# Kernel optimization log

Measured on AMD Instinct MI355X. Metric: run time of the kernel, lower is better.

## Reference

```python
import jax, jax.numpy as jnp
import numpy as np

N = 50000      # nodes
E = 800000     # edges
IN = 128       # in_channels
HID = 64       # hidden_channels
HEADS = 4
OUT = 2        # out_channels


def setup_inputs() -> dict:
    key = jax.random.key(0)
    ks = jax.random.split(key, 14)
    p = lambda k, shape: 0.1 * jax.random.normal(k, shape, dtype=jnp.float32)
    x = jax.random.normal(ks[0], (N, IN), dtype=jnp.float32)
    edge_index = jax.random.randint(ks[1], (2, E), 0, N, dtype=jnp.int64)
    return {
        'x': x, 'edge_index': edge_index,
        'W1': p(ks[2], (IN, HEADS * HID)), 'a_src1': p(ks[3], (HEADS, HID)),
        'a_dst1': p(ks[4], (HEADS, HID)), 'b1': p(ks[5], (HEADS * HID,)),
        'W2': p(ks[6], (HEADS * HID, HID)), 'a_src2': p(ks[7], (1, HID)),
        'a_dst2': p(ks[8], (1, HID)), 'b2': p(ks[9], (HID,)),
        'Wm1': p(ks[10], (2 * HID, HID)), 'bm1': p(ks[11], (HID,)),
        'Wm2': p(ks[12], (HID, OUT)), 'bm2': p(ks[13], (OUT,)),
    }


def _gat_conv(x, src, dst, W, a_src, a_dst, b, heads, out_c, concat):
    """PyG GATConv (eval mode): linear -> per-edge leakyrelu score ->
    segment softmax over destination -> scatter-sum aggregation."""
    n = x.shape[0]
    h = (x @ W).reshape(n, heads, out_c)                 # [N,H,C]
    s_src = jnp.einsum('nhc,hc->nh', h, a_src)           # [N,H]
    s_dst = jnp.einsum('nhc,hc->nh', h, a_dst)           # [N,H]
    e = jax.nn.leaky_relu(s_src[src] + s_dst[dst], 0.2)  # [E,H]
    m = jax.ops.segment_max(e, dst, num_segments=n)      # per-dst max (self-loops => no empty segs)
    ex = jnp.exp(e - m[dst])
    denom = jax.ops.segment_sum(ex, dst, num_segments=n)
    alpha = ex / (denom[dst] + 1e-16)                    # [E,H]
    out = jax.ops.segment_sum(h[src] * alpha[:, :, None], dst, num_segments=n)  # [N,H,C]
    if concat:
        return out.reshape(n, heads * out_c) + b
    return out.mean(axis=1) + b


def reference(x, edge_index, W1, a_src1, a_dst1, b1, W2, a_src2, a_dst2, b2,
              Wm1, bm1, Wm2, bm2):
    n = x.shape[0]
    loop = jnp.arange(n, dtype=edge_index.dtype)
    # GATConv add_self_loops=True (default)
    src = jnp.concatenate([edge_index[0], loop])
    dst = jnp.concatenate([edge_index[1], loop])
    h1 = jax.nn.relu(_gat_conv(x, src, dst, W1, a_src1, a_dst1, b1, HEADS, HID, True))
    h2 = _gat_conv(h1, src, dst, W2, a_src2, a_dst2, b2, 1, HID, False)   # [N,HID]
    parents, children = edge_index[0], edge_index[1]
    ef = jnp.concatenate([h2[parents], h2[children]], axis=1)             # [E,2*HID]
    return jax.nn.relu(ef @ Wm1 + bm1) @ Wm2 + bm2                        # [E,OUT]
```

## Files before the change

### kernel.cpp

```cpp
#include <hip/hip_runtime.h>
#include <hip/hip_fp16.h>

#define NN 50000
#define EE 800000
#define ENE (EE + NN)

typedef _Float16 f16;
typedef __attribute__((ext_vector_type(8))) _Float16 f16x8;
typedef __attribute__((ext_vector_type(4))) _Float16 f16x4;
typedef __attribute__((ext_vector_type(2))) _Float16 f16x2;
typedef __attribute__((ext_vector_type(4))) float f32x4;


__global__ __launch_bounds__(256)
void deg_kernel(const int* __restrict__ ei, int* __restrict__ deg) {
    int i = blockIdx.x * 256 + threadIdx.x;
    if (i >= ENE) return;
    int d = (i < EE) ? ei[EE + i] : (i - EE);
    atomicAdd(&deg[d], 1);
}

__global__ __launch_bounds__(1024)
void scan1_kernel(const int* __restrict__ deg, int* __restrict__ offs,
                  int* __restrict__ bsum) {
    __shared__ int s[1024];
    int t = threadIdx.x;
    int i = blockIdx.x * 1024 + t;
    int v = (i < NN) ? deg[i] : 0;
    s[t] = v;
    __syncthreads();
    for (int off = 1; off < 1024; off <<= 1) {
        int a = (t >= off) ? s[t - off] : 0;
        __syncthreads();
        s[t] += a;
        __syncthreads();
    }
    if (i < NN) offs[i] = s[t] - v;
    if (t == 1023) bsum[blockIdx.x] = s[1023];
}

__global__ __launch_bounds__(64)
void scan2_kernel(const int* __restrict__ bsum, int* __restrict__ bpre, int nb) {
    if (threadIdx.x == 0) {
        int run = 0;
        for (int b = 0; b < nb; ++b) { bpre[b] = run; run += bsum[b]; }
    }
}

__global__ __launch_bounds__(256)
void scan3_kernel(int* __restrict__ offs, const int* __restrict__ bpre) {
    int i = blockIdx.x * 256 + threadIdx.x;
    if (i >= NN) return;
    offs[i] += bpre[i >> 10];
}

__global__ __launch_bounds__(256)
void scatter_p1_kernel(const int* __restrict__ ei, int* __restrict__ offs,
                       int* __restrict__ csr_src, int* __restrict__ csr_dst,
                       const float* __restrict__ ss, const float* __restrict__ sd,
                       float4* __restrict__ p1) {
    int i = blockIdx.x * 256 + threadIdx.x;
    if (i >= ENE) return;
    int d, s;
    if (i < EE) { s = ei[i]; d = ei[EE + i]; }
    else        { s = i - EE; d = i - EE; }
    int slot = atomicAdd(&offs[d], 1);
    csr_src[slot] = s;
    csr_dst[slot] = d;
    float4 a = *(const float4*)&ss[s * 4];
    float4 b = *(const float4*)&sd[d * 4];
    float e0 = a.x + b.x; e0 = e0 > 0.f ? e0 : 0.2f * e0;
    float e1 = a.y + b.y; e1 = e1 > 0.f ? e1 : 0.2f * e1;
    float e2 = a.z + b.z; e2 = e2 > 0.f ? e2 : 0.2f * e2;
    float e3 = a.w + b.w; e3 = e3 > 0.f ? e3 : 0.2f * e3;
    p1[slot] = make_float4(__expf(e0), __expf(e1), __expf(e2), __expf(e3));
}


__global__ __launch_bounds__(256)
void cast_w_kernel(const float* __restrict__ W1, const float* __restrict__ W2,
                   const float* __restrict__ Wm1, f16* __restrict__ W1t,
                   f16* __restrict__ W2t, f16* __restrict__ Wmt) {
    int idx = blockIdx.x * 256 + threadIdx.x;
    if (idx < 32768) {
        int j = idx >> 7, k = idx & 127;
        W1t[idx] = (f16)W1[k * 256 + j];
    } else if (idx < 49152) {
        int i = idx - 32768;
        int j = i >> 8, k = i & 255;
        W2t[i] = (f16)W2[k * 64 + j];
    } else if (idx < 57344) {
        int i = idx - 49152;
        int j = i >> 6, k = i & 63;
        float v = (j < 64) ? Wm1[k * 64 + j] : Wm1[(64 + k) * 64 + (j - 64)];
        Wmt[i] = (f16)v;
    }
}


template<int K, int NOUT, int NWR, int NWC, int PERM, int AF32, int SCORES>
__global__ __launch_bounds__(256)
void mfma_gemm(const void* __restrict__ Avoid, const f16* __restrict__ Bt,
               f16* __restrict__ Yh, const float* __restrict__ a_src,
               const float* __restrict__ a_dst, float* __restrict__ ss,
               float* __restrict__ sd, int nrows) {
    constexpr int BROWS = NWR * 16;
    constexpr int LDP = NOUT + 8;
    __shared__ f16 lds[BROWS * LDP];
    const int tid = threadIdx.x;
    const int wid = tid >> 6, lane = tid & 63;
    const int wr = wid / NWC, wc = wid % NWC;
    const int lm = lane & 15, lk = lane >> 4;
    const int row0 = blockIdx.x * BROWS + wr * 16;
    const int col0 = wc * 64;

    const float* A32 = (const float*)Avoid;
    const f16*   A16 = (const f16*)Avoid;

    int arow = row0 + lm;
    if (arow >= nrows) arow = nrows - 1;

    f32x4 acc[4] = {};
#pragma unroll
    for (int ks = 0; ks < K / 32; ++ks) {
        f16x8 af;
        if (AF32) {
            float4 v0 = *(const float4*)&A32[(size_t)arow * K + ks * 32 + lk * 8];
            float4 v1 = *(const float4*)&A32[(size_t)arow * K + ks * 32 + lk * 8 + 4];
            af = f16x8{(f16)v0.x, (f16)v0.y, (f16)v0.z, (f16)v0.w,
                       (f16)v1.x, (f16)v1.y, (f16)v1.z, (f16)v1.w};
        } else {
            af = *(const f16x8*)(A16 + (size_t)arow * K + ks * 32 + lk * 8);
        }
#pragma unroll
        for (int ct = 0; ct < 4; ++ct) {
            const f16* bptr = Bt + (size_t)(col0 + ct * 16 + lm) * K + ks * 32 + lk * 8;
            f16x8 bf = *(const f16x8*)bptr;
            acc[ct] = __builtin_amdgcn_mfma_f32_16x16x32_f16(af, bf, acc[ct], 0, 0, 0);
        }
    }

#pragma unroll
    for (int ct = 0; ct < 4; ++ct) {
#pragma unroll
        for (int r = 0; r < 4; ++r) {
            int lrow = wr * 16 + lk * 4 + r;
            int j = col0 + ct * 16 + lm;
            int jj = PERM ? ((j & 63) * 4 + (j >> 6)) : j;
            lds[lrow * LDP + jj] = (f16)acc[ct][r];
        }
    }
    __syncthreads();

    constexpr int CHUNKS = NOUT / 8;
    for (int idx = tid; idx < BROWS * CHUNKS; idx += 256) {
        int lrow = idx / CHUNKS, ch = idx % CHUNKS;
        int grow = blockIdx.x * BROWS + lrow;
        if (grow < nrows) {
            f16x8 v = *(const f16x8*)&lds[lrow * LDP + ch * 8];
            *(f16x8*)&Yh[(size_t)grow * NOUT + ch * 8] = v;
        }
    }

    if (SCORES == 1) {
        int rloc = wid * 4 + (lane >> 4);
        int ci = lane & 15;
        float ps[4] = {}, pd[4] = {};
#pragma unroll
        for (int cc = 0; cc < 4; ++cc) {
            int c = ci + cc * 16;
            f16x4 hv = *(const f16x4*)&lds[rloc * LDP + c * 4];
#pragma unroll
            for (int h = 0; h < 4; ++h) {
                float f = (float)hv[h];
                ps[h] += f * a_src[h * 64 + c];
                pd[h] += f * a_dst[h * 64 + c];
            }
        }
#pragma unroll
        for (int m = 1; m < 16; m <<= 1) {
#pragma unroll
            for (int h = 0; h < 4; ++h) {
                ps[h] += __shfl_xor(ps[h], m);
                pd[h] += __shfl_xor(pd[h], m);
            }
        }
        if (ci == 0) {
            int grow = blockIdx.x * BROWS + rloc;
            if (grow < nrows) {
                *(float4*)&ss[grow * 4] = make_float4(ps[0], ps[1], ps[2], ps[3]);
                *(float4*)&sd[grow * 4] = make_float4(pd[0], pd[1], pd[2], pd[3]);
            }
        }
    } else if (SCORES == 2) {
        int rloc = wid * 16 + (lane >> 2);
        int cg = lane & 3;
        float ps = 0.f, pd = 0.f;
#pragma unroll
        for (int b = 0; b < 2; ++b) {
            f16x8 hv = *(const f16x8*)&lds[rloc * LDP + cg * 16 + b * 8];
#pragma unroll
            for (int u = 0; u < 8; ++u) {
                int c = cg * 16 + b * 8 + u;
                float f = (float)hv[u];
                ps += f * a_src[c];
                pd += f * a_dst[c];
            }
        }
        ps += __shfl_xor(ps, 1); ps += __shfl_xor(ps, 2);
        pd += __shfl_xor(pd, 1); pd += __shfl_xor(pd, 2);
        if (cg == 0) {
            int grow = blockIdx.x * BROWS + rloc;
            if (grow < nrows) { ss[grow] = ps; sd[grow] = pd; }
        }
    }
}


__global__ __launch_bounds__(256)
void p2_kernel(const int* __restrict__ csr_src, const int* __restrict__ csr_dst,
               const float* __restrict__ ss, const float* __restrict__ sd,
               float* __restrict__ p2) {
    int j = blockIdx.x * 256 + threadIdx.x;
    if (j >= ENE) return;
    float e = ss[csr_src[j]] + sd[csr_dst[j]];
    e = e > 0.f ? e : 0.2f * e;
    p2[j] = __expf(e);
}


__global__ __launch_bounds__(256)
void agg1_kernel(const int* __restrict__ offs, const int* __restrict__ csr_src,
                 const float4* __restrict__ p1, const f16* __restrict__ h1h,
                 const float* __restrict__ b1, f16* __restrict__ h1half) {
    int lane = threadIdx.x & 63;
    int hw = lane >> 5;
    int l = lane & 31;
    int n = blockIdx.x * 4 + (threadIdx.x >> 6);
    if (n >= NN) return;
    int beg = (n == 0) ? 0 : offs[n - 1];
    int end = offs[n];

    float den0 = 0.f, den1 = 0.f, den2 = 0.f, den3 = 0.f;
    float aA0 = 0.f, aA1 = 0.f, aA2 = 0.f, aA3 = 0.f;
    float aB0 = 0.f, aB1 = 0.f, aB2 = 0.f, aB3 = 0.f;
    int j = beg + hw;

#define AGG1_BODY(JJ)                                                          \
    {                                                                          \
        int s_ = csr_src[JJ];                                                  \
        float4 q_ = p1[JJ];                                                    \
        f16x8 hv_ = *(const f16x8*)&h1h[(size_t)s_ * 256 + l * 8];             \
        den0 += q_.x; den1 += q_.y; den2 += q_.z; den3 += q_.w;                \
        aA0 += q_.x * (float)hv_[0]; aB0 += q_.x * (float)hv_[4];              \
        aA1 += q_.y * (float)hv_[1]; aB1 += q_.y * (float)hv_[5];              \
        aA2 += q_.z * (float)hv_[2]; aB2 += q_.z * (float)hv_[6];              \
        aA3 += q_.w * (float)hv_[3]; aB3 += q_.w * (float)hv_[7];              \
    }

    for (; j + 6 < end; j += 8) {
        int s0 = csr_src[j + 0];
        int s1 = csr_src[j + 2];
        int s2 = csr_src[j + 4];
        int s3 = csr_src[j + 6];
        float4 q0 = p1[j + 0];
        float4 q1 = p1[j + 2];
        float4 q2 = p1[j + 4];
        float4 q3 = p1[j + 6];
        f16x8 h0 = *(const f16x8*)&h1h[(size_t)s0 * 256 + l * 8];
        f16x8 h1v = *(const f16x8*)&h1h[(size_t)s1 * 256 + l * 8];
        f16x8 h2v = *(const f16x8*)&h1h[(size_t)s2 * 256 + l * 8];
        f16x8 h3v = *(const f16x8*)&h1h[(size_t)s3 * 256 + l * 8];
        den0 += (q0.x + q1.x) + (q2.x + q3.x);
        den1 += (q0.y + q1.y) + (q2.y + q3.y);
        den2 += (q0.z + q1.z) + (q2.z + q3.z);
        den3 += (q0.w + q1.w) + (q2.w + q3.w);
        aA0 += q0.x * (float)h0[0] + q1.x * (float)h1v[0]
             + q2.x * (float)h2v[0] + q3.x * (float)h3v[0];
        aB0 += q0.x * (float)h0[4] + q1.x * (float)h1v[4]
             + q2.x * (float)h2v[4] + q3.x * (float)h3v[4];
        aA1 += q0.y * (float)h0[1] + q1.y * (float)h1v[1]
             + q2.y * (float)h2v[1] + q3.y * (float)h3v[1];
        aB1 += q0.y * (float)h0[5] + q1.y * (float)h1v[5]
             + q2.y * (float)h2v[5] + q3.y * (float)h3v[5];
        aA2 += q0.z * (float)h0[2] + q1.z * (float)h1v[2]
             + q2.z * (float)h2v[2] + q3.z * (float)h3v[2];
        aB2 += q0.z * (float)h0[6] + q1.z * (float)h1v[6]
             + q2.z * (float)h2v[6] + q3.z * (float)h3v[6];
        aA3 += q0.w * (float)h0[3] + q1.w * (float)h1v[3]
             + q2.w * (float)h2v[3] + q3.w * (float)h3v[3];
        aB3 += q0.w * (float)h0[7] + q1.w * (float)h1v[7]
             + q2.w * (float)h2v[7] + q3.w * (float)h3v[7];
    }
    for (; j < end; j += 2) AGG1_BODY(j);
#undef AGG1_BODY

    den0 += __shfl_xor(den0, 32); den1 += __shfl_xor(den1, 32);
    den2 += __shfl_xor(den2, 32); den3 += __shfl_xor(den3, 32);
    aA0 += __shfl_xor(aA0, 32);   aB0 += __shfl_xor(aB0, 32);
    aA1 += __shfl_xor(aA1, 32);   aB1 += __shfl_xor(aB1, 32);
    aA2 += __shfl_xor(aA2, 32);   aB2 += __shfl_xor(aB2, 32);
    aA3 += __shfl_xor(aA3, 32);   aB3 += __shfl_xor(aB3, 32);

    if (hw == 0) {
        f16* orow = &h1half[(size_t)n * 256];
        float i0 = 1.f / (den0 + 1e-16f);
        float i1 = 1.f / (den1 + 1e-16f);
        float i2 = 1.f / (den2 + 1e-16f);
        float i3 = 1.f / (den3 + 1e-16f);
        float2 bb0 = *(const float2*)&b1[0 * 64 + 2 * l];
        float2 bb1 = *(const float2*)&b1[1 * 64 + 2 * l];
        float2 bb2 = *(const float2*)&b1[2 * 64 + 2 * l];
        float2 bb3 = *(const float2*)&b1[3 * 64 + 2 * l];
        float rA, rB;
        rA = aA0 * i0 + bb0.x; rB = aB0 * i0 + bb0.y;
        *(f16x2*)&orow[0 * 64 + 2 * l] = f16x2{(f16)(rA > 0.f ? rA : 0.f), (f16)(rB > 0.f ? rB : 0.f)};
        rA = aA1 * i1 + bb1.x; rB = aB1 * i1 + bb1.y;
        *(f16x2*)&orow[1 * 64 + 2 * l] = f16x2{(f16)(rA > 0.f ? rA : 0.f), (f16)(rB > 0.f ? rB : 0.f)};
        rA = aA2 * i2 + bb2.x; rB = aB2 * i2 + bb2.y;
        *(f16x2*)&orow[2 * 64 + 2 * l] = f16x2{(f16)(rA > 0.f ? rA : 0.f), (f16)(rB > 0.f ? rB : 0.f)};
        rA = aA3 * i3 + bb3.x; rB = aB3 * i3 + bb3.y;
        *(f16x2*)&orow[3 * 64 + 2 * l] = f16x2{(f16)(rA > 0.f ? rA : 0.f), (f16)(rB > 0.f ? rB : 0.f)};
    }
}

__global__ __launch_bounds__(256)
void agg2_kernel(const int* __restrict__ offs, const int* __restrict__ csr_src,
                 const float* __restrict__ p2, const f16* __restrict__ h2linh,
                 const float* __restrict__ b2, f16* __restrict__ h2half) {
    int lane = threadIdx.x & 63;
    int hw = lane >> 5;
    int l = lane & 31;
    int n = blockIdx.x * 4 + (threadIdx.x >> 6);
    if (n >= NN) return;
    int beg = (n == 0) ? 0 : offs[n - 1];
    int end = offs[n];

    float den = 0.f, aA = 0.f, aB = 0.f;
    int j = beg + hw;
    for (; j + 6 < end; j += 8) {
        int s0 = csr_src[j + 0];
        int s1 = csr_src[j + 2];
        int s2 = csr_src[j + 4];
        int s3 = csr_src[j + 6];
        float q0 = p2[j + 0];
        float q1 = p2[j + 2];
        float q2 = p2[j + 4];
        float q3 = p2[j + 6];
        f16x2 v0 = *(const f16x2*)&h2linh[(size_t)s0 * 64 + l * 2];
        f16x2 v1 = *(const f16x2*)&h2linh[(size_t)s1 * 64 + l * 2];
        f16x2 v2 = *(const f16x2*)&h2linh[(size_t)s2 * 64 + l * 2];
        f16x2 v3 = *(const f16x2*)&h2linh[(size_t)s3 * 64 + l * 2];
        den += (q0 + q1) + (q2 + q3);
        aA += q0 * (float)v0[0] + q1 * (float)v1[0]
            + q2 * (float)v2[0] + q3 * (float)v3[0];
        aB += q0 * (float)v0[1] + q1 * (float)v1[1]
            + q2 * (float)v2[1] + q3 * (float)v3[1];
    }
    for (; j < end; j += 2) {
        int s = csr_src[j];
        float q = p2[j];
        f16x2 v = *(const f16x2*)&h2linh[(size_t)s * 64 + l * 2];
        den += q;
        aA += q * (float)v[0];
        aB += q * (float)v[1];
    }

    den += __shfl_xor(den, 32);
    aA  += __shfl_xor(aA, 32);
    aB  += __shfl_xor(aB, 32);

    if (hw == 0) {
        float inv = 1.f / (den + 1e-16f);
        float2 bb = *(const float2*)&b2[2 * l];
        f16x2 o = f16x2{(f16)(aA * inv + bb.x), (f16)(aB * inv + bb.y)};
        *(f16x2*)&h2half[(size_t)n * 64 + 2 * l] = o;
    }
}


__global__ __launch_bounds__(256)
void edge_kernel(const int* __restrict__ ei, const f16* __restrict__ gh,
                 const float* __restrict__ bm1, const float* __restrict__ Wm2,
                 const float* __restrict__ bm2, float* __restrict__ out) {
    int l = threadIdx.x & 15;
    int eid = blockIdx.x * 16 + (threadIdx.x >> 4);
    if (eid >= EE) return;
    int p = ei[eid];
    int c = ei[EE + eid];
    f16x4 av = *(const f16x4*)&gh[(size_t)p * 128 + l * 4];
    f16x4 bv = *(const f16x4*)&gh[(size_t)c * 128 + 64 + l * 4];
    float4 bb = *(const float4*)&bm1[l * 4];
    float zx = (float)av[0] + (float)bv[0] + bb.x; zx = zx > 0.f ? zx : 0.f;
    float zy = (float)av[1] + (float)bv[1] + bb.y; zy = zy > 0.f ? zy : 0.f;
    float zz = (float)av[2] + (float)bv[2] + bb.z; zz = zz > 0.f ? zz : 0.f;
    float zw = (float)av[3] + (float)bv[3] + bb.w; zw = zw > 0.f ? zw : 0.f;
    float4 w01 = *(const float4*)&Wm2[l * 8];
    float4 w23 = *(const float4*)&Wm2[l * 8 + 4];
    float o0 = zx * w01.x + zy * w01.z + zz * w23.x + zw * w23.z;
    float o1 = zx * w01.y + zy * w01.w + zz * w23.y + zw * w23.w;
#pragma unroll
    for (int m = 1; m < 16; m <<= 1) {
        o0 += __shfl_xor(o0, m);
        o1 += __shfl_xor(o1, m);
    }
    if (l == 0)
        *(float2*)&out[(size_t)eid * 2] = make_float2(o0 + bm2[0], o1 + bm2[1]);
}


extern "C" void kernel_launch(void* const* d_in, const int* in_sizes, int n_in,
                              void* d_out, int out_size, void* d_ws, size_t ws_size,
                              hipStream_t stream) {
    const float* x      = (const float*)d_in[0];
    const int*   ei     = (const int*)d_in[1];
    const float* W1     = (const float*)d_in[2];
    const float* a_src1 = (const float*)d_in[3];
    const float* a_dst1 = (const float*)d_in[4];
    const float* b1     = (const float*)d_in[5];
    const float* W2     = (const float*)d_in[6];
    const float* a_src2 = (const float*)d_in[7];
    const float* a_dst2 = (const float*)d_in[8];
    const float* b2     = (const float*)d_in[9];
    const float* Wm1    = (const float*)d_in[10];
    const float* bm1    = (const float*)d_in[11];
    const float* Wm2    = (const float*)d_in[12];
    const float* bm2    = (const float*)d_in[13];
    float* out = (float*)d_out;

    char* ws = (char*)d_ws;
    size_t off = 0;
    auto alloc = [&](size_t bytes) -> void* {
        void* p = ws + off;
        off += (bytes + 255) & ~(size_t)255;
        return p;
    };
    int*    deg     = (int*)alloc((size_t)NN * 4);
    int*    offs    = (int*)alloc((size_t)NN * 4);
    int*    bsum    = (int*)alloc(64 * 4);
    int*    bpre    = (int*)alloc(64 * 4);
    int*    csr_src = (int*)alloc((size_t)ENE * 4);
    int*    csr_dst = (int*)alloc((size_t)ENE * 4);
    float*  ss1     = (float*)alloc((size_t)NN * 4 * 4);
    float*  sd1     = (float*)alloc((size_t)NN * 4 * 4);
    float*  ss2     = (float*)alloc((size_t)NN * 4);
    float*  sd2     = (float*)alloc((size_t)NN * 4);
    float4* p1      = (float4*)alloc((size_t)ENE * 16);
    float*  p2      = (float*)alloc((size_t)ENE * 4);
    f16*    W1t     = (f16*)alloc((size_t)256 * 128 * 2);
    f16*    W2t     = (f16*)alloc((size_t)64 * 256 * 2);
    f16*    Wmt     = (f16*)alloc((size_t)128 * 64 * 2);
    f16*    h1h     = (f16*)alloc((size_t)NN * 256 * 2);
    f16*    h1half  = (f16*)alloc((size_t)NN * 256 * 2);
    f16*    h2linh  = (f16*)alloc((size_t)NN * 64 * 2);
    f16*    h2half  = (f16*)alloc((size_t)NN * 64 * 2);
    f16*    gh      = (f16*)alloc((size_t)NN * 128 * 2);
    if (off > ws_size) return;

    const int nbScan  = (NN + 1023) / 1024;
    const int gEdges  = (ENE + 255) / 256;
    const int gNodes4 = (NN + 3) / 4;
    const int gEdge16 = (EE + 15) / 16;

    cast_w_kernel<<<(57344 + 255) / 256, 256, 0, stream>>>(W1, W2, Wm1, W1t, W2t, Wmt);

    hipMemsetAsync(deg, 0, (size_t)NN * 4, stream);
    deg_kernel<<<gEdges, 256, 0, stream>>>(ei, deg);
    scan1_kernel<<<nbScan, 1024, 0, stream>>>(deg, offs, bsum);
    scan2_kernel<<<1, 64, 0, stream>>>(bsum, bpre, nbScan);
    scan3_kernel<<<(NN + 255) / 256, 256, 0, stream>>>(offs, bpre);

    mfma_gemm<128, 256, 1, 4, 1, 1, 1><<<NN / 16, 256, 0, stream>>>(
        x, W1t, h1h, a_src1, a_dst1, ss1, sd1, NN);

    scatter_p1_kernel<<<gEdges, 256, 0, stream>>>(ei, offs, csr_src, csr_dst,
                                                  ss1, sd1, p1);
    agg1_kernel<<<gNodes4, 256, 0, stream>>>(offs, csr_src, p1, h1h, b1, h1half);

    mfma_gemm<256, 64, 4, 1, 0, 0, 2><<<(NN + 63) / 64, 256, 0, stream>>>(
        h1half, W2t, h2linh, a_src2, a_dst2, ss2, sd2, NN);
    p2_kernel<<<gEdges, 256, 0, stream>>>(csr_src, csr_dst, ss2, sd2, p2);
    agg2_kernel<<<gNodes4, 256, 0, stream>>>(offs, csr_src, p2, h2linh, b2, h2half);

    mfma_gemm<64, 128, 2, 2, 0, 0, 0><<<(NN + 31) / 32, 256, 0, stream>>>(
        h2half, Wmt, gh, nullptr, nullptr, nullptr, nullptr, NN);
    edge_kernel<<<gEdge16, 256, 0, stream>>>(ei, gh, bm1, Wm2, bm2, out);
}
```

Measured before the change: 406.8 us.

## Fuse layer-2 edge score into agg2 and widen edge MLP per-thread vectors

Removes the separate p2 kernel and the csr_dst array: agg2 now computes the leaky-relu/exp score per edge inline from ss2[src] and sd2[n], which avoids writing and re-reading an E-sized p2 buffer and csr_dst. The scatter kernel no longer stores csr_dst. Separately, the edge MLP kernel now uses 8 lanes per edge with 8-wide f16 loads instead of 16 lanes with 4-wide loads, which halves the shuffle reduction depth and processes more edges per block. The trade-off is redundant exp work across the 32 lanes that share each edge in agg2, plus an extra random gather of ss2.

New measurement: 392.8 us. 1.04x faster.

```diff
diff --git a/kernel.cpp b/kernel.cpp
--- a/kernel.cpp
+++ b/kernel.cpp
@@ -56,7 +56,7 @@
 
 __global__ __launch_bounds__(256)
 void scatter_p1_kernel(const int* __restrict__ ei, int* __restrict__ offs,
-                       int* __restrict__ csr_src, int* __restrict__ csr_dst,
+                       int* __restrict__ csr_src,
                        const float* __restrict__ ss, const float* __restrict__ sd,
                        float4* __restrict__ p1) {
     int i = blockIdx.x * 256 + threadIdx.x;
@@ -66,7 +66,6 @@
     else        { s = i - EE; d = i - EE; }
     int slot = atomicAdd(&offs[d], 1);
     csr_src[slot] = s;
-    csr_dst[slot] = d;
     float4 a = *(const float4*)&ss[s * 4];
     float4 b = *(const float4*)&sd[d * 4];
     float e0 = a.x + b.x; e0 = e0 > 0.f ? e0 : 0.2f * e0;
@@ -214,18 +213,6 @@
             if (grow < nrows) { ss[grow] = ps; sd[grow] = pd; }
         }
     }
-}
-
-
-__global__ __launch_bounds__(256)
-void p2_kernel(const int* __restrict__ csr_src, const int* __restrict__ csr_dst,
-               const float* __restrict__ ss, const float* __restrict__ sd,
-               float* __restrict__ p2) {
-    int j = blockIdx.x * 256 + threadIdx.x;
-    if (j >= ENE) return;
-    float e = ss[csr_src[j]] + sd[csr_dst[j]];
-    e = e > 0.f ? e : 0.2f * e;
-    p2[j] = __expf(e);
 }
 
 
@@ -326,7 +313,8 @@
 
 __global__ __launch_bounds__(256)
 void agg2_kernel(const int* __restrict__ offs, const int* __restrict__ csr_src,
-                 const float* __restrict__ p2, const f16* __restrict__ h2linh,
+                 const float* __restrict__ ss, const float* __restrict__ sd,
+                 const f16* __restrict__ h2linh,
                  const float* __restrict__ b2, f16* __restrict__ h2half) {
     int lane = threadIdx.x & 63;
     int hw = lane >> 5;
@@ -335,6 +323,7 @@
     if (n >= NN) return;
     int beg = (n == 0) ? 0 : offs[n - 1];
     int end = offs[n];
+    float sdn = sd[n];
 
     float den = 0.f, aA = 0.f, aB = 0.f;
     int j = beg + hw;
@@ -343,14 +332,22 @@
         int s1 = csr_src[j + 2];
         int s2 = csr_src[j + 4];
         int s3 = csr_src[j + 6];
-        float q0 = p2[j + 0];
-        float q1 = p2[j + 2];
-        float q2 = p2[j + 4];
-        float q3 = p2[j + 6];
+        float e0 = ss[s0] + sdn;
+        float e1 = ss[s1] + sdn;
+        float e2 = ss[s2] + sdn;
+        float e3 = ss[s3] + sdn;
         f16x2 v0 = *(const f16x2*)&h2linh[(size_t)s0 * 64 + l * 2];
         f16x2 v1 = *(const f16x2*)&h2linh[(size_t)s1 * 64 + l * 2];
         f16x2 v2 = *(const f16x2*)&h2linh[(size_t)s2 * 64 + l * 2];
         f16x2 v3 = *(const f16x2*)&h2linh[(size_t)s3 * 64 + l * 2];
+        e0 = e0 > 0.f ? e0 : 0.2f * e0;
+        e1 = e1 > 0.f ? e1 : 0.2f * e1;
+        e2 = e2 > 0.f ? e2 : 0.2f * e2;
+        e3 = e3 > 0.f ? e3 : 0.2f * e3;
+        float q0 = __expf(e0);
+        float q1 = __expf(e1);
+        float q2 = __expf(e2);
+        float q3 = __expf(e3);
         den += (q0 + q1) + (q2 + q3);
         aA += q0 * (float)v0[0] + q1 * (float)v1[0]
             + q2 * (float)v2[0] + q3 * (float)v3[0];
@@ -359,7 +356,9 @@
     }
     for (; j < end; j += 2) {
         int s = csr_src[j];
-        float q = p2[j];
+        float e = ss[s] + sdn;
+        e = e > 0.f ? e : 0.2f * e;
+        float q = __expf(e);
         f16x2 v = *(const f16x2*)&h2linh[(size_t)s * 64 + l * 2];
         den += q;
         aA += q * (float)v[0];
@@ -383,24 +382,33 @@
 void edge_kernel(const int* __restrict__ ei, const f16* __restrict__ gh,
                  const float* __restrict__ bm1, const float* __restrict__ Wm2,
                  const float* __restrict__ bm2, float* __restrict__ out) {
-    int l = threadIdx.x & 15;
-    int eid = blockIdx.x * 16 + (threadIdx.x >> 4);
+    int l = threadIdx.x & 7;
+    int eid = blockIdx.x * 32 + (threadIdx.x >> 3);
     if (eid >= EE) return;
     int p = ei[eid];
     int c = ei[EE + eid];
-    f16x4 av = *(const f16x4*)&gh[(size_t)p * 128 + l * 4];
-    f16x4 bv = *(const f16x4*)&gh[(size_t)c * 128 + 64 + l * 4];
-    float4 bb = *(const float4*)&bm1[l * 4];
-    float zx = (float)av[0] + (float)bv[0] + bb.x; zx = zx > 0.f ? zx : 0.f;
-    float zy = (float)av[1] + (float)bv[1] + bb.y; zy = zy > 0.f ? zy : 0.f;
-    float zz = (float)av[2] + (float)bv[2] + bb.z; zz = zz > 0.f ? zz : 0.f;
-    float zw = (float)av[3] + (float)bv[3] + bb.w; zw = zw > 0.f ? zw : 0.f;
-    float4 w01 = *(const float4*)&Wm2[l * 8];
-    float4 w23 = *(const float4*)&Wm2[l * 8 + 4];
-    float o0 = zx * w01.x + zy * w01.z + zz * w23.x + zw * w23.z;
-    float o1 = zx * w01.y + zy * w01.w + zz * w23.y + zw * w23.w;
-#pragma unroll
-    for (int m = 1; m < 16; m <<= 1) {
+    f16x8 av = *(const f16x8*)&gh[(size_t)p * 128 + l * 8];
+    f16x8 bv = *(const f16x8*)&gh[(size_t)c * 128 + 64 + l * 8];
+    float4 bb0 = *(const float4*)&bm1[l * 8];
+    float4 bb1 = *(const float4*)&bm1[l * 8 + 4];
+    float z0 = (float)av[0] + (float)bv[0] + bb0.x; z0 = z0 > 0.f ? z0 : 0.f;
+    float z1 = (float)av[1] + (float)bv[1] + bb0.y; z1 = z1 > 0.f ? z1 : 0.f;
+    float z2 = (float)av[2] + (float)bv[2] + bb0.z; z2 = z2 > 0.f ? z2 : 0.f;
+    float z3 = (float)av[3] + (float)bv[3] + bb0.w; z3 = z3 > 0.f ? z3 : 0.f;
+    float z4 = (float)av[4] + (float)bv[4] + bb1.x; z4 = z4 > 0.f ? z4 : 0.f;
+    float z5 = (float)av[5] + (float)bv[5] + bb1.y; z5 = z5 > 0.f ? z5 : 0.f;
+    float z6 = (float)av[6] + (float)bv[6] + bb1.z; z6 = z6 > 0.f ? z6 : 0.f;
+    float z7 = (float)av[7] + (float)bv[7] + bb1.w; z7 = z7 > 0.f ? z7 : 0.f;
+    float4 w01 = *(const float4*)&Wm2[l * 16];
+    float4 w23 = *(const float4*)&Wm2[l * 16 + 4];
+    float4 w45 = *(const float4*)&Wm2[l * 16 + 8];
+    float4 w67 = *(const float4*)&Wm2[l * 16 + 12];
+    float o0 = z0 * w01.x + z1 * w01.z + z2 * w23.x + z3 * w23.z
+             + z4 * w45.x + z5 * w45.z + z6 * w67.x + z7 * w67.z;
+    float o1 = z0 * w01.y + z1 * w01.w + z2 * w23.y + z3 * w23.w
+             + z4 * w45.y + z5 * w45.w + z6 * w67.y + z7 * w67.w;
+#pragma unroll
+    for (int m = 1; m < 8; m <<= 1) {
         o0 += __shfl_xor(o0, m);
         o1 += __shfl_xor(o1, m);
     }
@@ -440,13 +448,11 @@
     int*    bsum    = (int*)alloc(64 * 4);
     int*    bpre    = (int*)alloc(64 * 4);
     int*    csr_src = (int*)alloc((size_t)ENE * 4);
-    int*    csr_dst = (int*)alloc((size_t)ENE * 4);
     float*  ss1     = (float*)alloc((size_t)NN * 4 * 4);
     float*  sd1     = (float*)alloc((size_t)NN * 4 * 4);
     float*  ss2     = (float*)alloc((size_t)NN * 4);
     float*  sd2     = (float*)alloc((size_t)NN * 4);
     float4* p1      = (float4*)alloc((size_t)ENE * 16);
-    float*  p2      = (float*)alloc((size_t)ENE * 4);
     f16*    W1t     = (f16*)alloc((size_t)256 * 128 * 2);
     f16*    W2t     = (f16*)alloc((size_t)64 * 256 * 2);
     f16*    Wmt     = (f16*)alloc((size_t)128 * 64 * 2);
@@ -460,7 +466,7 @@
     const int nbScan  = (NN + 1023) / 1024;
     const int gEdges  = (ENE + 255) / 256;
     const int gNodes4 = (NN + 3) / 4;
-    const int gEdge16 = (EE + 15) / 16;
+    const int gEdge32 = (EE + 31) / 32;
 
     cast_w_kernel<<<(57344 + 255) / 256, 256, 0, stream>>>(W1, W2, Wm1, W1t, W2t, Wmt);
 
@@ -473,16 +479,14 @@
     mfma_gemm<128, 256, 1, 4, 1, 1, 1><<<NN / 16, 256, 0, stream>>>(
         x, W1t, h1h, a_src1, a_dst1, ss1, sd1, NN);
 
-    scatter_p1_kernel<<<gEdges, 256, 0, stream>>>(ei, offs, csr_src, csr_dst,
-                                                  ss1, sd1, p1);
+    scatter_p1_kernel<<<gEdges, 256, 0, stream>>>(ei, offs, csr_src, ss1, sd1, p1);
     agg1_kernel<<<gNodes4, 256, 0, stream>>>(offs, csr_src, p1, h1h, b1, h1half);
 
     mfma_gemm<256, 64, 4, 1, 0, 0, 2><<<(NN + 63) / 64, 256, 0, stream>>>(
         h1half, W2t, h2linh, a_src2, a_dst2, ss2, sd2, NN);
-    p2_kernel<<<gEdges, 256, 0, stream>>>(csr_src, csr_dst, ss2, sd2, p2);
-    agg2_kernel<<<gNodes4, 256, 0, stream>>>(offs, csr_src, p2, h2linh, b2, h2half);
+    agg2_kernel<<<gNodes4, 256, 0, stream>>>(offs, csr_src, ss2, sd2, h2linh, b2, h2half);
 
     mfma_gemm<64, 128, 2, 2, 0, 0, 0><<<(NN + 31) / 32, 256, 0, stream>>>(
         h2half, Wmt, gh, nullptr, nullptr, nullptr, nullptr, NN);
-    edge_kernel<<<gEdge16, 256, 0, stream>>>(ei, gh, bm1, Wm2, bm2, out);
-}
+    edge_kernel<<<gEdge32, 256, 0, stream>>>(ei, gh, bm1, Wm2, bm2, out);
+}
```
